# Optimization experiments

Hardware: AMD Instinct MI355X
Metric: run time of the kernel (lower is better)

## Reference

```python
import jax
jax.config.update("jax_enable_x64", True)
import jax.numpy as jnp
import numpy as np

SIGMA_2 = 0.1  # SNR = 10 dB -> sigma^2 = 1/10^(10/10)
P = 1.0        # total transmit power

NT, NR, DK, KU, BR = 64, 4, 2, 8, 16
BATCH = 256


def setup_inputs() -> dict:
    key = jax.random.key(0)
    k1, k2 = jax.random.split(key)
    channel = jax.random.normal(k1, (BATCH, NT * NR * BR * 2 * KU), dtype=jnp.float32)
    pred_w = 2 * NR * DK * KU * BR + DK * DK * KU * BR  # 2560
    prediction = jax.random.normal(k2, (BATCH, pred_w), dtype=jnp.float32)
    return {"channel": channel, "prediction": prediction,
            "Nt": NT, "Nr": NR, "dk": DK, "K": KU, "B": BR}


def reference(channel, prediction, Nt, Nr, dk, K, B):
    # --- unpack complex channel: [b, Nt, Nr, B, 2K] -> [b, Nr, Nt, B, K] complex
    Hc = channel.reshape(-1, Nt, Nr, B, 2 * K).astype(jnp.complex128)
    H = Hc[..., :K] + 1j * Hc[..., K:]
    H = jnp.transpose(H, (0, 2, 1, 3, 4))  # [b, Nr, Nt, B, K]

    nu = 2 * Nr * dk * K * B
    u_flat = prediction[:, :nu]
    w_flat = prediction[:, nu:nu + dk * dk * K * B]
    Uc = u_flat.reshape(-1, Nr, dk, B, 2 * K).astype(jnp.complex128)
    U = Uc[..., :K] + 1j * Uc[..., K:]           # [b, Nr, dk, B, K]
    W = w_flat.reshape(-1, dk, dk, B, K).astype(jnp.complex128)  # real-valued W

    # HHU[b,:,:,f,k] = H^H U  -> [b, Nt, dk, B, K]
    HHU = jnp.einsum('brtfk,brdfk->btdfk', jnp.conj(H), U)

    # sum over (rb, user) of sigma2/p * trace(U W U^H)
    tr_UWU = (SIGMA_2 / P) * jnp.einsum('brdfk,bdefk,brefk->b', U, W, jnp.conj(U))
    # sum over (rb, user) of (H^H U) W (H^H U)^H  -> [b, Nt, Nt]
    quad = jnp.einsum('btdfk,bdefk,bsefk->bts', HHU, W, jnp.conj(HHU))
    temp_B = quad + tr_UWU[:, None, None] * jnp.eye(Nt, dtype=jnp.complex128)
    temp_B_inv = jnp.linalg.inv(temp_B)  # batched Nt x Nt complex inverse

    # HUW[b,:,:,k] = sum_rb (H^H U) W  -> [b, Nt, dk, K]
    HUW = jnp.einsum('btdfk,bdefk->btek', HHU, W)
    V0 = jnp.einsum('bts,bsdk->btdk', temp_B_inv, HUW)  # [b, Nt, dk, K]

    # l2-normalize flattened precoder per sample (tf.linalg.normalize)
    flat = V0.reshape(-1, Nt * dk * K)
    flat = flat / jnp.linalg.norm(flat, axis=1, keepdims=True)
    V0 = flat.reshape(-1, Nt, dk, K)

    # power normalization: trace(sum_k V_k V_k^H)
    trace_VV = jnp.einsum('btdk,btdk->b', V0, jnp.conj(V0))
    scale = jnp.sqrt(P / jnp.real(trace_VV).astype(jnp.float32))
    V = V0 * scale.astype(jnp.complex128)[:, None, None, None]

    V = V.reshape(-1, Nt, dk, K, 1)
    return jnp.concatenate([jnp.real(V), jnp.imag(V)], axis=4).astype(jnp.float32)
```

## Files before the change

kernel.cpp:

```cpp
#include <hip/hip_runtime.h>
#include <math.h>


#define SAUG 84
#define STP  65

namespace {
union alignas(16) ShU {
    struct { float4 TtP[2][2][8][STP]; float4 HtP[2][2][8][STP]; } p1;
    float2 Aug[64][SAUG];
};
union alignas(16) ShV {
    struct { float2 U[4 * 258]; float W[512]; } in;
    float2 xout[64][17];
};
}

__device__ __forceinline__ float2 cmul(float2 x, float2 y) {
    return make_float2(x.x * y.x - x.y * y.y, x.x * y.y + x.y * y.x);
}

__global__ __launch_bounds__(512, 1)
void uw2v_kernel(const float* __restrict__ channel,
                 const float* __restrict__ prediction,
                 float2* __restrict__ out)
{
    __shared__ ShU sh;
    __shared__ ShV sv;
    __shared__ alignas(16) float2 pivR[2][8][80];
    __shared__ float2 pivI[2][8];
    __shared__ float2 redbuf[8];
    __shared__ float  fred[8];

    const int b   = blockIdx.x;
    const int tid = threadIdx.x;
    const int wv  = tid >> 6;
    const float* pred = prediction + (size_t)b * 2560;
    const float* chan = channel + (size_t)b * 65536;

    #pragma unroll
    for (int i = 0; i < 2; ++i) {
        int m = tid + i * 512;
        int r = m >> 8, d = (m >> 7) & 1, f = (m >> 3) & 15, k = m & 7;
        const float* src = pred + (((r * 2 + d) * 16 + f) << 4);
        sv.in.U[r * 258 + ((d * 16 + f) << 3) + k] = make_float2(src[k], src[k + 8]);
    }
    sv.in.W[tid] = pred[2048 + tid];
    __syncthreads();

    const int half = tid >> 8;
    const int lt   = tid & 255;
    const int t4 = lt >> 2, r4 = lt & 3;
    const int a  = lt >> 4, bb = lt & 15;
    const int bit0 = r4 & 1, bit1 = (r4 >> 1) & 1;
    const int kkb  = 4 * bit0 + 2 * bit1;
    const int mpb  = kkb >> 1;
    const int fbase = half << 3;
    const int tr_r = lt >> 5, tr_d = (lt >> 4) & 1, tr_e = (lt >> 3) & 1, tr_k = lt & 7;

    float2 accA[4][4], accB[4][4];
    #pragma unroll
    for (int i = 0; i < 4; ++i)
        #pragma unroll
        for (int j = 0; j < 4; ++j) {
            accA[i][j] = make_float2(0.f, 0.f);
            accB[i][j] = make_float2(0.f, 0.f);
        }
    float2 huw[4] = {make_float2(0,0), make_float2(0,0), make_float2(0,0), make_float2(0,0)};
    float2 tracc  = make_float2(0.f, 0.f);

    const float* hbase = chan + ((t4 * 4 + r4) << 8) + (fbase << 4);

    #pragma unroll 1
    for (int fi = 0; fi < 8; ++fi) {
        const int f = fbase + fi;
        const float4 ca = *(const float4*)(hbase + (fi << 4) + 0);
        const float4 cb = *(const float4*)(hbase + (fi << 4) + 4);
        const float4 ci = *(const float4*)(hbase + (fi << 4) + 8);
        const float4 cd = *(const float4*)(hbase + (fi << 4) + 12);

        const float4* U0p = (const float4*)&sv.in.U[r4 * 258 + (f << 3)];
        const float4* U1p = (const float4*)&sv.in.U[r4 * 258 + ((16 + f) << 3)];
        const float4 u0q0 = U0p[0], u0q1 = U0p[1], u0q2 = U0p[2], u0q3 = U0p[3];
        const float4 u1q0 = U1p[0], u1q1 = U1p[1], u1q2 = U1p[2], u1q3 = U1p[3];

        float2 val0[8], val1[8];
        #define MK2(K, HR, HI, U0R, U0I, U1R, U1I) \
            val0[K] = make_float2((HR)*(U0R) + (HI)*(U0I), (HR)*(U0I) - (HI)*(U0R)); \
            val1[K] = make_float2((HR)*(U1R) + (HI)*(U1I), (HR)*(U1I) - (HI)*(U1R));
        MK2(0, ca.x, ci.x, u0q0.x, u0q0.y, u1q0.x, u1q0.y)
        MK2(1, ca.y, ci.y, u0q0.z, u0q0.w, u1q0.z, u1q0.w)
        MK2(2, ca.z, ci.z, u0q1.x, u0q1.y, u1q1.x, u1q1.y)
        MK2(3, ca.w, ci.w, u0q1.z, u0q1.w, u1q1.z, u1q1.w)
        MK2(4, cb.x, cd.x, u0q2.x, u0q2.y, u1q2.x, u1q2.y)
        MK2(5, cb.y, cd.y, u0q2.z, u0q2.w, u1q2.z, u1q2.w)
        MK2(6, cb.z, cd.z, u0q3.x, u0q3.y, u1q3.x, u1q3.y)
        MK2(7, cb.w, cd.w, u0q3.z, u0q3.w, u1q3.z, u1q3.w)
        #undef MK2

        float2 s1d0[4], s1d1[4];
        #pragma unroll
        for (int q = 0; q < 4; ++q) {
            float2 k0 = bit0 ? val0[4 + q] : val0[q];
            float2 n0 = bit0 ? val0[q]     : val0[4 + q];
            float2 k1 = bit0 ? val1[4 + q] : val1[q];
            float2 n1 = bit0 ? val1[q]     : val1[4 + q];
            n0.x = __shfl_xor(n0.x, 1); n0.y = __shfl_xor(n0.y, 1);
            n1.x = __shfl_xor(n1.x, 1); n1.y = __shfl_xor(n1.y, 1);
            s1d0[q] = make_float2(k0.x + n0.x, k0.y + n0.y);
            s1d1[q] = make_float2(k1.x + n1.x, k1.y + n1.y);
        }
        float2 h0[2], h1[2];
        #pragma unroll
        for (int jj = 0; jj < 2; ++jj) {
            float2 k0 = bit1 ? s1d0[2 + jj] : s1d0[jj];
            float2 n0 = bit1 ? s1d0[jj]     : s1d0[2 + jj];
            float2 k1 = bit1 ? s1d1[2 + jj] : s1d1[jj];
            float2 n1 = bit1 ? s1d1[jj]     : s1d1[2 + jj];
            n0.x = __shfl_xor(n0.x, 2); n0.y = __shfl_xor(n0.y, 2);
            n1.x = __shfl_xor(n1.x, 2); n1.y = __shfl_xor(n1.y, 2);
            h0[jj] = make_float2(k0.x + n0.x, k0.y + n0.y);
            h1[jj] = make_float2(k1.x + n1.x, k1.y + n1.y);
        }

        if (lt < 128) {
            float w   = sv.in.W[((tr_d * 2 + tr_e) * 16 + f) * 8 + tr_k];
            float2 u1 = sv.in.U[tr_r * 258 + ((tr_d * 16 + f) << 3) + tr_k];
            float2 u2 = sv.in.U[tr_r * 258 + ((tr_e * 16 + f) << 3) + tr_k];
            tracc.x += w * (u1.x * u2.x + u1.y * u2.y);
            tracc.y += w * (u1.y * u2.x - u1.x * u2.y);
        }

        const int p = fi & 1;
        #pragma unroll
        for (int e = 0; e < 2; ++e) {
            float w0a = sv.in.W[(e * 16 + f) * 8 + kkb];
            float w0b = sv.in.W[(e * 16 + f) * 8 + kkb + 1];
            float w1a = sv.in.W[((2 + e) * 16 + f) * 8 + kkb];
            float w1b = sv.in.W[((2 + e) * 16 + f) * 8 + kkb + 1];
            float2 tva = make_float2(h0[0].x * w0a + h1[0].x * w1a,
                                     h0[0].y * w0a + h1[0].y * w1a);
            float2 tvb = make_float2(h0[1].x * w0b + h1[1].x * w1b,
                                     h0[1].y * w0b + h1[1].y * w1b);
            sh.p1.TtP[p][half][e * 4 + mpb][t4] = make_float4(tva.x, tva.y, tvb.x, tvb.y);
            huw[e * 2 + 0].x += tva.x; huw[e * 2 + 0].y += tva.y;
            huw[e * 2 + 1].x += tvb.x; huw[e * 2 + 1].y += tvb.y;
        }
        sh.p1.HtP[p][half][mpb][t4]     = make_float4(h0[0].x, h0[0].y, h0[1].x, h0[1].y);
        sh.p1.HtP[p][half][4 + mpb][t4] = make_float4(h1[0].x, h1[0].y, h1[1].x, h1[1].y);
        __syncthreads();

        #pragma unroll
        for (int mp = 0; mp < 8; ++mp) {
            float4 tq[4], hq[4];
            #pragma unroll
            for (int i = 0; i < 4; ++i) tq[i] = sh.p1.TtP[p][half][mp][a + 16 * i];
            #pragma unroll
            for (int j = 0; j < 4; ++j) hq[j] = sh.p1.HtP[p][half][mp][bb + 16 * j];
            #pragma unroll
            for (int i = 0; i < 4; ++i)
                #pragma unroll
                for (int j = 0; j < 4; ++j) {
                    float2 va = accA[i][j], vb = accB[i][j];
                    va.x = fmaf(tq[i].x, hq[j].x, va.x);
                    va.y = fmaf(tq[i].x, hq[j].y, va.y);
                    vb.x = fmaf(tq[i].y, hq[j].x, vb.x);
                    vb.y = fmaf(tq[i].y, hq[j].y, vb.y);
                    va.x = fmaf(tq[i].z, hq[j].z, va.x);
                    va.y = fmaf(tq[i].z, hq[j].w, va.y);
                    vb.x = fmaf(tq[i].w, hq[j].z, vb.x);
                    vb.y = fmaf(tq[i].w, hq[j].w, vb.y);
                    accA[i][j] = va; accB[i][j] = vb;
                }
        }
    }

    #pragma unroll
    for (int off = 32; off; off >>= 1) {
        tracc.x += __shfl_xor(tracc.x, off);
        tracc.y += __shfl_xor(tracc.y, off);
    }
    if ((tid & 63) == 0) redbuf[wv] = tracc;
    __syncthreads();
    float2 trv = make_float2(0.f, 0.f);
    #pragma unroll
    for (int w = 0; w < 8; ++w) { trv.x += redbuf[w].x; trv.y += redbuf[w].y; }
    trv.x *= 0.1f; trv.y *= 0.1f;

    if (half == 0) {
        #pragma unroll
        for (int i = 0; i < 4; ++i)
            #pragma unroll
            for (int j = 0; j < 4; ++j) {
                float2 v = make_float2(accA[i][j].x + accB[i][j].y,
                                       accB[i][j].x - accA[i][j].y);
                int row = a + 16 * i, col = bb + 16 * j;
                if (row == col) { v.x += trv.x; v.y += trv.y; }
                sh.Aug[row][col] = v;
            }
        #pragma unroll
        for (int e = 0; e < 2; ++e)
            #pragma unroll
            for (int jj = 0; jj < 2; ++jj)
                sh.Aug[t4][64 + e * 8 + kkb + jj] = huw[e * 2 + jj];
    }
    __syncthreads();
    if (half == 1) {
        #pragma unroll
        for (int i = 0; i < 4; ++i)
            #pragma unroll
            for (int j = 0; j < 4; ++j) {
                int row = a + 16 * i, col = bb + 16 * j;
                float2 v = sh.Aug[row][col];
                v.x += accA[i][j].x + accB[i][j].y;
                v.y += accB[i][j].x - accA[i][j].y;
                sh.Aug[row][col] = v;
            }
        #pragma unroll
        for (int e = 0; e < 2; ++e)
            #pragma unroll
            for (int jj = 0; jj < 2; ++jj) {
                int col = 64 + e * 8 + kkb + jj;
                float2 v = sh.Aug[t4][col];
                v.x += huw[e * 2 + jj].x; v.y += huw[e * 2 + jj].y;
                sh.Aug[t4][col] = v;
            }
    }
    __syncthreads();

    const int gi = tid >> 3, gc = tid & 7;
    const int cb = 10 * gc;
    const int lanebase = (tid & 63) & 56;

    float2 xr[10];
    {
        const float4* rp = (const float4*)&sh.Aug[gi][cb];
        float4 q0 = rp[0], q1 = rp[1], q2 = rp[2], q3 = rp[3], q4 = rp[4];
        xr[0] = make_float2(q0.x, q0.y); xr[1] = make_float2(q0.z, q0.w);
        xr[2] = make_float2(q1.x, q1.y); xr[3] = make_float2(q1.z, q1.w);
        xr[4] = make_float2(q2.x, q2.y); xr[5] = make_float2(q2.z, q2.w);
        xr[6] = make_float2(q3.x, q3.y); xr[7] = make_float2(q3.z, q3.w);
        xr[8] = make_float2(q4.x, q4.y); xr[9] = make_float2(q4.z, q4.w);
    }

    float2 myipv = make_float2(0.f, 0.f);

    auto cascade = [&](int chunk, int nb) {
        #pragma unroll
        for (int p = 0; p < 8; ++p) {
            const int col = 8 * chunk + p;
            const int cs  = col / 10;
            float2 cand = make_float2(0.f, 0.f);
            #pragma unroll
            for (int c = 0; c < 10; ++c)
                if (cb + c == col) cand = xr[c];
            float2 z, Lv;
            z.x  = __shfl(cand.x, p * 8 + cs);
            z.y  = __shfl(cand.y, p * 8 + cs);
            Lv.x = __shfl(cand.x, lanebase + cs);
            Lv.y = __shfl(cand.y, lanebase + cs);
            float  zi  = 1.0f / (z.x * z.x + z.y * z.y);
            float2 ipv = make_float2(z.x * zi, -z.y * zi);
            const bool isPiv = (gi == col);
            if (isPiv) myipv = ipv;
            float2 pr[10];
            #pragma unroll
            for (int c = 0; c < 10; ++c) {
                pr[c].x = __shfl(xr[c].x, p * 8 + gc);
                pr[c].y = __shfl(xr[c].y, p * 8 + gc);
            }
            if (!isPiv) {
                float2 L = cmul(Lv, ipv);
                #pragma unroll
                for (int c = 0; c < 10; ++c) {
                    xr[c].x -= L.x * pr[c].x - L.y * pr[c].y;
                    xr[c].y -= L.x * pr[c].y + L.y * pr[c].x;
                }
            }
        }
        const int prw = gi & 7;
        float4* wp = (float4*)&pivR[nb][prw][cb];
        wp[0] = make_float4(xr[0].x, xr[0].y, xr[1].x, xr[1].y);
        wp[1] = make_float4(xr[2].x, xr[2].y, xr[3].x, xr[3].y);
        wp[2] = make_float4(xr[4].x, xr[4].y, xr[5].x, xr[5].y);
        wp[3] = make_float4(xr[6].x, xr[6].y, xr[7].x, xr[7].y);
        wp[4] = make_float4(xr[8].x, xr[8].y, xr[9].x, xr[9].y);
        if (gc == 0) pivI[nb][prw] = myipv;
    };

    auto eliminate = [&](int chunk, int bf) {
        #pragma unroll
        for (int p = 0; p < 8; ++p) {
            const int col = 8 * chunk + p;
            float2 cand = make_float2(0.f, 0.f);
            #pragma unroll
            for (int c = 0; c < 10; ++c)
                if (cb + c == col) cand = xr[c];
            float2 Lv;
            Lv.x = __shfl(cand.x, lanebase + col / 10);
            Lv.y = __shfl(cand.y, lanebase + col / 10);
            float2 ipv = pivI[bf][p];
            float2 L = cmul(Lv, ipv);
            const float4* pp = (const float4*)&pivR[bf][p][cb];
            float4 p0 = pp[0], p1 = pp[1], p2 = pp[2], p3 = pp[3], p4 = pp[4];
            float2 pr[10];
            pr[0] = make_float2(p0.x, p0.y); pr[1] = make_float2(p0.z, p0.w);
            pr[2] = make_float2(p1.x, p1.y); pr[3] = make_float2(p1.z, p1.w);
            pr[4] = make_float2(p2.x, p2.y); pr[5] = make_float2(p2.z, p2.w);
            pr[6] = make_float2(p3.x, p3.y); pr[7] = make_float2(p3.z, p3.w);
            pr[8] = make_float2(p4.x, p4.y); pr[9] = make_float2(p4.z, p4.w);
            #pragma unroll
            for (int c = 0; c < 10; ++c) {
                xr[c].x -= L.x * pr[c].x - L.y * pr[c].y;
                xr[c].y -= L.x * pr[c].y + L.y * pr[c].x;
            }
        }
    };

    int cur = 0;
    if (wv == 0) cascade(0, 0);
    __syncthreads();

    #pragma unroll 1
    for (int c = 0; c < 8; ++c) {
        if (wv != c) {
            eliminate(c, cur);
            if (wv == c + 1) cascade(c + 1, cur ^ 1);
        }
        __syncthreads();
        cur ^= 1;
    }

    float ss = 0.f;
    if (gc == 6) {
        #pragma unroll
        for (int c = 4; c < 10; ++c) {
            float2 xv = cmul(xr[c], myipv);
            ss += xv.x * xv.x + xv.y * xv.y;
            sv.xout[gi][c - 4] = xv;
        }
    } else if (gc == 7) {
        #pragma unroll
        for (int c = 0; c < 10; ++c) {
            float2 xv = cmul(xr[c], myipv);
            ss += xv.x * xv.x + xv.y * xv.y;
            sv.xout[gi][6 + c] = xv;
        }
    }
    #pragma unroll
    for (int off = 32; off; off >>= 1) ss += __shfl_xor(ss, off);
    if ((tid & 63) == 0) fred[wv] = ss;
    __syncthreads();
    float total = 0.f;
    #pragma unroll
    for (int w = 0; w < 8; ++w) total += fred[w];
    float invn = rsqrtf(total);
    #pragma unroll
    for (int q = 0; q < 2; ++q) {
        int m = tid + q * 512;
        float2 v = sv.xout[m >> 4][m & 15];
        out[(size_t)b * 1024 + m] = make_float2(v.x * invn, v.y * invn);
    }
}

extern "C" void kernel_launch(void* const* d_in, const int* in_sizes, int n_in,
                              void* d_out, int out_size, void* d_ws, size_t ws_size,
                              hipStream_t stream) {
    const float* channel    = (const float*)d_in[0];
    const float* prediction = (const float*)d_in[1];
    int batch = in_sizes[0] / 65536;
    uw2v_kernel<<<dim3(batch), dim3(512), 0, stream>>>(channel, prediction,
                                                       (float2*)d_out);
}
```

Baseline: 166.2 us.

## Prefetch channel tiles into LDS via async global_load_lds double buffering

Replaces the per-iteration direct global float4 loads of the channel with asynchronous global-to-LDS loads into a double buffer. The next frequency slice is issued before the barrier and outer-product phase, so the load overlaps compute. The LDS buffer is unioned with the Gauss-Jordan pivot storage, and synchronisation now uses explicit waitcnt plus s_barrier. The risks are added LDS traffic and the correctness of the manual wait counts.

Result: no change. 166.9 us (+0.5%).

```diff
diff --git a/kernel.cpp b/kernel.cpp
--- a/kernel.cpp
+++ b/kernel.cpp
@@ -14,6 +14,10 @@
     struct { float2 U[4 * 258]; float W[512]; } in;
     float2 xout[64][17];
 };
+union alignas(16) ShC {
+    float4 chBuf[2][8][4][64];
+    struct { float2 pivR[2][8][80]; float2 pivI[2][8]; } gj;
+};
 }
 
 __device__ __forceinline__ float2 cmul(float2 x, float2 y) {
@@ -27,14 +31,14 @@
 {
     __shared__ ShU sh;
     __shared__ ShV sv;
-    __shared__ alignas(16) float2 pivR[2][8][80];
-    __shared__ float2 pivI[2][8];
+    __shared__ ShC shc;
     __shared__ float2 redbuf[8];
     __shared__ float  fred[8];
 
     const int b   = blockIdx.x;
     const int tid = threadIdx.x;
     const int wv  = tid >> 6;
+    const int lane = tid & 63;
     const float* pred = prediction + (size_t)b * 2560;
     const float* chan = channel + (size_t)b * 65536;
 
@@ -71,13 +75,25 @@
 
     const float* hbase = chan + ((t4 * 4 + r4) << 8) + (fbase << 4);
 
-    #pragma unroll 1
-    for (int fi = 0; fi < 8; ++fi) {
+    auto issueL = [&](int fi, int n) {
+        #pragma unroll
+        for (int k = 0; k < 4; ++k) {
+            const float* g = hbase + (fi << 4) + (k << 2);
+            __builtin_amdgcn_global_load_lds(
+                (const __attribute__((address_space(1))) void*)g,
+                (__attribute__((address_space(3))) void*)&shc.chBuf[n][wv][k][0],
+                16, 0, 0);
+        }
+    };
+
+    auto stage = [&](int fi, int c, int p) {
         const int f = fbase + fi;
-        const float4 ca = *(const float4*)(hbase + (fi << 4) + 0);
-        const float4 cb = *(const float4*)(hbase + (fi << 4) + 4);
-        const float4 ci = *(const float4*)(hbase + (fi << 4) + 8);
-        const float4 cd = *(const float4*)(hbase + (fi << 4) + 12);
+        asm volatile("s_waitcnt vmcnt(0)" ::: "memory");
+        __builtin_amdgcn_sched_barrier(0);
+        const float4 ca = shc.chBuf[c][wv][0][lane];
+        const float4 cb = shc.chBuf[c][wv][1][lane];
+        const float4 ci = shc.chBuf[c][wv][2][lane];
+        const float4 cd = shc.chBuf[c][wv][3][lane];
 
         const float4* U0p = (const float4*)&sv.in.U[r4 * 258 + (f << 3)];
         const float4* U1p = (const float4*)&sv.in.U[r4 * 258 + ((16 + f) << 3)];
@@ -131,7 +147,6 @@
             tracc.y += w * (u1.y * u2.x - u1.x * u2.y);
         }
 
-        const int p = fi & 1;
         #pragma unroll
         for (int e = 0; e < 2; ++e) {
             float w0a = sv.in.W[(e * 16 + f) * 8 + kkb];
@@ -148,8 +163,9 @@
         }
         sh.p1.HtP[p][half][mpb][t4]     = make_float4(h0[0].x, h0[0].y, h0[1].x, h0[1].y);
         sh.p1.HtP[p][half][4 + mpb][t4] = make_float4(h1[0].x, h1[0].y, h1[1].x, h1[1].y);
-        __syncthreads();
-
+    };
+
+    auto quadf = [&](int p) {
         #pragma unroll
         for (int mp = 0; mp < 8; ++mp) {
             float4 tq[4], hq[4];
@@ -173,6 +189,22 @@
                     accA[i][j] = va; accB[i][j] = vb;
                 }
         }
+    };
+
+    auto rbar = [&]() {
+        asm volatile("s_waitcnt lgkmcnt(0)" ::: "memory");
+        __builtin_amdgcn_s_barrier();
+        asm volatile("" ::: "memory");
+    };
+
+    issueL(0, 0);
+    #pragma unroll 1
+    for (int fi = 0; fi < 8; ++fi) {
+        const int p = fi & 1;
+        stage(fi, p, p);
+        if (fi < 7) issueL(fi + 1, p ^ 1);
+        rbar();
+        quadf(p);
     }
 
     #pragma unroll
@@ -279,13 +311,13 @@
             }
         }
         const int prw = gi & 7;
-        float4* wp = (float4*)&pivR[nb][prw][cb];
+        float4* wp = (float4*)&shc.gj.pivR[nb][prw][cb];
         wp[0] = make_float4(xr[0].x, xr[0].y, xr[1].x, xr[1].y);
         wp[1] = make_float4(xr[2].x, xr[2].y, xr[3].x, xr[3].y);
         wp[2] = make_float4(xr[4].x, xr[4].y, xr[5].x, xr[5].y);
         wp[3] = make_float4(xr[6].x, xr[6].y, xr[7].x, xr[7].y);
         wp[4] = make_float4(xr[8].x, xr[8].y, xr[9].x, xr[9].y);
-        if (gc == 0) pivI[nb][prw] = myipv;
+        if (gc == 0) shc.gj.pivI[nb][prw] = myipv;
     };
 
     auto eliminate = [&](int chunk, int bf) {
@@ -299,9 +331,9 @@
             float2 Lv;
             Lv.x = __shfl(cand.x, lanebase + col / 10);
             Lv.y = __shfl(cand.y, lanebase + col / 10);
-            float2 ipv = pivI[bf][p];
+            float2 ipv = shc.gj.pivI[bf][p];
             float2 L = cmul(Lv, ipv);
-            const float4* pp = (const float4*)&pivR[bf][p][cb];
+            const float4* pp = (const float4*)&shc.gj.pivR[bf][p][cb];
             float4 p0 = pp[0], p1 = pp[1], p2 = pp[2], p3 = pp[3], p4 = pp[4];
             float2 pr[10];
             pr[0] = make_float2(p0.x, p0.y); pr[1] = make_float2(p0.z, p0.w);
```
